# Kernel tuning notes

Measured on AMD Instinct MI355X. Metric: run time of the kernel, lower is better.

The kernel has to match this reference:

```python
import jax, jax.numpy as jnp
import numpy as np
from math import pi

RADIUS = 40.0  # radius_scale
B, N = 1, 512


def map_polar_sqr(x, y, eps=1e-9):
    r = jnp.sqrt(x * x + y * y + eps)
    cond1 = (x == 0.0) & (y == 0.0)
    cond2 = (jnp.abs(y) <= jnp.abs(x)) & (~cond1)
    sx = jnp.where(x == 0.0, 1.0, x)  # safe denominators
    sy = jnp.where(y == 0.0, 1.0, y)
    c = 4.0 / pi
    x2 = jnp.sign(x) * r
    y2 = c * jnp.sign(x) * r * jnp.arctan(y / sx)
    x3 = c * jnp.sign(y) * r * jnp.arctan(x / sy)
    y3 = jnp.sign(y) * r
    x_out = jnp.where(cond1, 0.0, jnp.where(cond2, x2, x3))
    y_out = jnp.where(cond1, 0.0, jnp.where(cond2, y2, y3))
    return x_out, y_out


def axis_weights(g, size):
    # F.grid_sample bilinear, align_corners=False, padding_mode='zeros':
    # pixel coord = ((g+1)*size - 1)/2; linear weights on floor/floor+1,
    # out-of-range taps drop to zero automatically (idx only covers 0..size-1).
    c = ((g + 1.0) * size - 1.0) * 0.5
    i0 = jnp.floor(c)
    f = c - i0
    idx = jnp.arange(size, dtype=g.dtype)
    m0 = (idx == i0[..., None]).astype(g.dtype)
    m1 = (idx == i0[..., None] + 1.0).astype(g.dtype)
    return (1.0 - f)[..., None] * m0 + f[..., None] * m1  # [..., size]


def cts_conv(kernel, field, center, feat, mask, radius):
    # kernel: [o, i, kD, kH, kW]; field/center: [b, n/m, 3]; feat: [b, n, i]; mask: [b, n, 1]
    rel = (field[:, None] - center[:, :, None]) / radius            # [b,m,n,3]
    r2 = jnp.sum(rel * rel, -1)                                     # [b,m,n]
    att = jax.nn.relu((1.0 - r2) ** 3)[..., None] * mask[:, None]   # [b,m,n,1]
    xs, ys = map_polar_sqr(rel[..., 0], rel[..., 1])
    zs = rel[..., 2]
    kD, kH, kW = kernel.shape[2:]
    # grid_sample coord order: grid x -> W (last dim), y -> H, z -> D (first spatial dim)
    wz = axis_weights(zs, kD)
    wy = axis_weights(ys, kH)
    wx = axis_weights(xs, kW)
    w = jnp.einsum('bmnz,bmny,bmnx->bmnzyx', wz, wy, wx)
    w = w.reshape(*w.shape[:3], -1)                                 # [b,m,n,g=kD*kH*kW]
    fa = feat[:, None] * att                                        # [b,m,n,i]
    # exact trilinear interp + neighbor contraction without the [b,m,n,o,i] tensor:
    t = jnp.einsum('bmng,bmni->bmgi', w, fa)                        # [b,m,g,i]
    K = kernel.reshape(kernel.shape[0], kernel.shape[1], -1)        # [o,i,g]
    return jnp.einsum('bmgi,oig->bmo', t, K)


def setup_inputs() -> dict:
    key = jax.random.key(0)
    ks = jax.random.split(key, 24)

    def kern(k, o, i):
        return (jax.random.uniform(k, (o, i, 4, 4, 4), dtype=jnp.float32) - 0.5) / float(np.sqrt(i))

    def lin(kw, kb, o, i):
        return (jax.random.normal(kw, (o, i), dtype=jnp.float32) * 0.05,
                jax.random.normal(kb, (o,), dtype=jnp.float32) * 0.05)

    p = jax.random.normal(ks[0], (B, N, 3), dtype=jnp.float32) * 20.0
    v = jax.random.normal(ks[1], (B, N, 3), dtype=jnp.float32)
    other_feats = jax.random.normal(ks[2], (B, N, 62), dtype=jnp.float32)
    fluid_mask = jnp.ones((B, N, 1), dtype=jnp.float32)

    k_fluid = kern(ks[3], 32, 66)
    Wf, bf = lin(ks[4], ks[5], 32, 66)
    k1 = kern(ks[6], 64, 64); W1, b1 = lin(ks[7], ks[8], 64, 64)
    k2 = kern(ks[9], 64, 64); W2, b2 = lin(ks[10], ks[11], 64, 64)
    k3 = kern(ks[12], 64, 64); W3, b3 = lin(ks[13], ks[14], 64, 64)
    k4 = kern(ks[15], 6, 64); W4, b4 = lin(ks[16], ks[17], 6, 64)
    return dict(p=p, v=v, other_feats=other_feats, fluid_mask=fluid_mask,
                k_fluid=k_fluid, Wf=Wf, bf=bf,
                k1=k1, W1=W1, b1=b1, k2=k2, W2=W2, b2=b2,
                k3=k3, W3=W3, b3=b3, k4=k4, W4=W4, b4=b4)


def reference(p, v, other_feats, fluid_mask, k_fluid, Wf, bf,
              k1, W1, b1, k2, W2, b2, k3, W3, b3, k4, W4, b4):
    feats0 = jnp.concatenate([jnp.ones_like(p[..., :1]), v, other_feats], -1)  # [b,n,66]
    oc = cts_conv(k_fluid, p, p, feats0, fluid_mask, RADIUS)
    od = feats0 @ Wf.T + bf
    output = jnp.concatenate([oc, od], -1)  # [b,n,64]
    for k, W, bb in ((k1, W1, b1), (k2, W2, b2), (k3, W3, b3), (k4, W4, b4)):
        h = jax.nn.relu(output)
        oc = cts_conv(k, p, p, h, fluid_mask, RADIUS)
        od = h @ W.T + bb
        if od.shape[-1] == output.shape[-1]:
            output = oc + od + output
        else:
            output = oc + od
    return output  # [b,n,6]
```

## Files before the change

kernel.cpp:

```cpp
#include <hip/hip_runtime.h>

typedef _Float16 f16;
typedef _Float16 f16x8 __attribute__((ext_vector_type(8)));
typedef float f32x4 __attribute__((ext_vector_type(4)));
typedef int iv2 __attribute__((ext_vector_type(2)));

#define INV_R (1.0f / 40.0f)
#define NBLK 512

#define F_BAR 0u
#define F_B0  2304u
#define F_K   2560u
#define F_HT  2286080u
#define F_T0  2695680u
#define F_T1  7119360u
#define F_T2  11379200u
#define F_T3  15639040u
#define F_T4  19898880u
#define F_OG  24158720u
#define NEED_FULL 24289792u

#define C_B0  2304u
#define C_K   2560u
#define C_HTA 2286080u
#define C_HTB 2368000u
#define C_TA  2449920u
#define C_TB  6873600u
#define C_OG  11133440u

#define K1_OFF 552960u
#define K2_OFF 1085440u
#define K3_OFF 1617920u
#define K4_OFF 2150400u

#define PREP_TOTAL 1231936

__device__ __forceinline__ void st_sys_u16(void* p, unsigned v) {
  asm volatile("global_store_short %0, %1, off sc0 sc1" :: "v"(p), "v"(v) : "memory");
}
__device__ __forceinline__ void st_sys_f32(float* p, float v) {
  asm volatile("global_store_dword %0, %1, off sc0 sc1" :: "v"(p), "v"(v) : "memory");
}
__device__ __forceinline__ void st_sys_b64(void* p, iv2 v) {
  asm volatile("global_store_dwordx2 %0, %1, off sc0 sc1" :: "v"(p), "v"(v) : "memory");
}
__device__ __forceinline__ unsigned f16bits(float x) {
  union { f16 h; unsigned short s; } cv; cv.h = (f16)x; return (unsigned)cv.s;
}

__device__ __forceinline__ unsigned bar_ld(unsigned* p) {
  return __hip_atomic_load(p, __ATOMIC_RELAXED, __HIP_MEMORY_SCOPE_AGENT);
}
__device__ void gridbar(unsigned* bar, int phase) {
  asm volatile("s_waitcnt vmcnt(0)" ::: "memory");
  __syncthreads();
  if (threadIdx.x == 0) {
    int bid = blockIdx.x;
    int xcd = bid & 7;
    unsigned* xcnt = bar + xcd * 32 + phase;
    unsigned* xrel = bar + 256 + xcd * 32 + phase;
    unsigned* gcnt = bar + 512 + phase;
    unsigned* grel = bar + 544 + phase;
    __hip_atomic_fetch_add(xcnt, 1u, __ATOMIC_RELAXED, __HIP_MEMORY_SCOPE_AGENT);
    if (bid < 8) {
      while (bar_ld(xcnt) < (NBLK / 8)) __builtin_amdgcn_s_sleep(2);
      __hip_atomic_fetch_add(gcnt, 1u, __ATOMIC_RELAXED, __HIP_MEMORY_SCOPE_AGENT);
      if (bid == 0) {
        while (bar_ld(gcnt) < 8u) __builtin_amdgcn_s_sleep(2);
        __hip_atomic_store(grel, 1u, __ATOMIC_RELAXED, __HIP_MEMORY_SCOPE_AGENT);
      } else {
        while (bar_ld(grel) == 0u) __builtin_amdgcn_s_sleep(4);
      }
      __hip_atomic_store(xrel, 1u, __ATOMIC_RELAXED, __HIP_MEMORY_SCOPE_AGENT);
    } else {
      while (bar_ld(xrel) == 0u) __builtin_amdgcn_s_sleep(64);
    }
    asm volatile("" ::: "memory");
  }
  __syncthreads();
}

__device__ __forceinline__ float feats0_val(int ch, int n, const float* v, const float* other) {
  if (ch == 0) return 1.0f;
  if (ch < 4) return v[n * 3 + (ch - 1)];
  return other[n * 62 + (ch - 4)];
}
__device__ __forceinline__ float atan_poly(float t) {
  float t2 = t * t;
  float p = -0.0117212f;
  p = p * t2 + 0.05265332f;
  p = p * t2 - 0.11643287f;
  p = p * t2 + 0.19354346f;
  p = p * t2 - 0.33262347f;
  p = p * t2 + 0.99997726f;
  return t * p;
}
__device__ __forceinline__ void axis_w(float g, int& i0c, int& i1c, float& w0, float& w1) {
  float c = 2.0f * g + 1.5f;
  float fl = floorf(c);
  float f = c - fl;
  int i0 = (int)fl;
  w0 = (i0 >= 0 && i0 <= 3) ? (1.0f - f) : 0.0f;
  w1 = (i0 >= -1 && i0 <= 2) ? f : 0.0f;
  i0c = min(max(i0, 0), 3);
  i1c = min(max(i0 + 1, 0), 3);
}

__device__ void prep_body(const float* __restrict__ v, const float* __restrict__ other,
                          const float* __restrict__ kf, const float* __restrict__ Wf,
                          const float* __restrict__ bf,
                          const float* __restrict__ k1, const float* __restrict__ W1,
                          const float* __restrict__ k2, const float* __restrict__ W2,
                          const float* __restrict__ k3, const float* __restrict__ W3,
                          const float* __restrict__ k4, const float* __restrict__ W4,
                          f16* __restrict__ K0, float* __restrict__ B0,
                          f16* __restrict__ hT0, f16* __restrict__ t0) {
  for (int idx = blockIdx.x * 256 + threadIdx.x; idx < PREP_TOTAL; idx += NBLK * 256) {
    int e = idx;
    if (e < 40960) {
      int i = e >> 9, n = e & 511;
      float val = (i < 66) ? feats0_val(i, n, v, other) : 0.0f;
      st_sys_u16(hT0 + e, f16bits(val));
      continue;
    }
    e -= 40960;
    if (e < 49152) {
      int m = e / 96, j = e % 96;
      float val = (j < 66) ? feats0_val(j, m, v, other) : 0.0f;
      st_sys_u16(t0 + (size_t)m * 4320 + 4224 + j, f16bits(val));
      continue;
    }
    e -= 49152;
    if (e < 276480) {
      int o = e / 4320, k = e % 4320;
      float val = 0.0f;
      if (o < 32) { if (k < 4224) val = kf[o * 4224 + k]; }
      else if (k >= 4224 && k < 4290) val = Wf[(o - 32) * 66 + (k - 4224)];
      st_sys_u16(K0 + e, f16bits(val));
      continue;
    }
    e -= 276480;
    if (e < 798720) {
      int which = e / 266240, ee = e % 266240;
      const float* kk = which == 0 ? k1 : (which == 1 ? k2 : k3);
      const float* WW = which == 0 ? W1 : (which == 1 ? W2 : W3);
      int o = ee / 4160, k = ee % 4160;
      float val = (k < 4096) ? kk[o * 4096 + k] : WW[o * 64 + (k - 4096)];
      st_sys_u16(K0 + (K1_OFF / 2) + (size_t)which * 266240 + ee, f16bits(val));
      continue;
    }
    e -= 798720;
    if (e < 66560) {
      int o = e / 4160, k = e % 4160;
      float val = 0.0f;
      if (o < 6) val = (k < 4096) ? k4[o * 4096 + k] : W4[o * 64 + (k - 4096)];
      st_sys_u16(K0 + (K4_OFF / 2) + e, f16bits(val));
      continue;
    }
    e -= 66560;
    if (e < 64) st_sys_f32(&B0[e], (e < 32) ? 0.0f : bf[e - 32]);
  }
}

template<int CI, int ITILES, int KDIM>
__device__ void stage1_body(const float* __restrict__ p, const float* __restrict__ mask,
                            const f16* __restrict__ hT_in, f16* __restrict__ tout,
                            f16* __restrict__ Wl) {
  const int tid = threadIdx.x;
  const int m = blockIdx.x;
  const int wave = tid >> 6, lane = tid & 63;
  const int row = lane & 15, kgrp = lane >> 4;
  const int grow = wave * 16 + row;

  const float pmx = p[m * 3 + 0], pmy = p[m * 3 + 1], pmz = p[m * 3 + 2];
  f32x4 acc[ITILES];
  #pragma unroll
  for (int it = 0; it < ITILES; ++it) acc[it] = f32x4{0.f, 0.f, 0.f, 0.f};

  #pragma unroll
  for (int half = 0; half < 2; ++half) {
    __syncthreads();
    int4* w4 = (int4*)Wl;
    int4 z4 = make_int4(0, 0, 0, 0);
    #pragma unroll
    for (int i = 0; i < 8; ++i) w4[tid + i * 256] = z4;
    __syncthreads();
    {
      const int n = half * 256 + tid;
      float x = (p[n * 3 + 0] - pmx) * INV_R;
      float y = (p[n * 3 + 1] - pmy) * INV_R;
      float z = (p[n * 3 + 2] - pmz) * INV_R;
      float r2 = x * x + y * y + z * z;
      float q = 1.0f - r2;
      float att = (q > 0.0f) ? q * q * q * mask[n] : 0.0f;
      bool c1 = (x == 0.0f) && (y == 0.0f);
      bool c2 = (fabsf(y) <= fabsf(x)) && !c1;
      float r = sqrtf(x * x + y * y + 1e-9f);
      float num = c2 ? y : x;
      float den = c2 ? x : y;
      float a = atan_poly(num / den);
      float s2 = copysignf(r, x), s3 = copysignf(r, y);
      const float C4PI = 1.2732395447351628f;
      float xs = c1 ? 0.0f : (c2 ? s2 : C4PI * s3 * a);
      float ys = c1 ? 0.0f : (c2 ? C4PI * s2 * a : s3);
      float zs = z;
      int iz0, iz1, iy0, iy1, ix0, ix1;
      float wz0, wz1, wy0, wy1, wx0, wx1;
      axis_w(zs, iz0, iz1, wz0, wz1);
      axis_w(ys, iy0, iy1, wy0, wy1);
      axis_w(xs, ix0, ix1, wx0, wx1);
      wz0 *= att; wz1 *= att;
      int gz[2] = {iz0 * 16, iz1 * 16};
      int gy[2] = {iy0 * 4, iy1 * 4};
      int gx[2] = {ix0, ix1};
      float wzv[2] = {wz0, wz1}, wyv[2] = {wy0, wy1}, wxv[2] = {wx0, wx1};
      #pragma unroll
      for (int za = 0; za < 2; ++za)
        #pragma unroll
        for (int ya = 0; ya < 2; ++ya)
          #pragma unroll
          for (int xa = 0; xa < 2; ++xa) {
            float w = wzv[za] * wyv[ya] * wxv[xa];
            if (w != 0.0f) {
              int g = gz[za] + gy[ya] + gx[xa];
              Wl[g * 256 + (tid ^ ((g & 7) << 3))] = (f16)w;
            }
          }
    }
    __syncthreads();
    #pragma unroll
    for (int k0 = 0; k0 < 8; ++k0) {
      const int n0l = k0 * 32 + kgrp * 8;
      f16x8 afrag = *(f16x8*)&Wl[grow * 256 + (n0l ^ ((grow & 7) << 3))];
      f16x8 bfr[ITILES];
      #pragma unroll
      for (int it = 0; it < ITILES; ++it)
        bfr[it] = *(const f16x8*)&hT_in[(it * 16 + row) * 512 + half * 256 + n0l];
      #pragma unroll
      for (int it = 0; it < ITILES; ++it)
        acc[it] = __builtin_amdgcn_mfma_f32_16x16x32_f16(afrag, bfr[it], acc[it], 0, 0, 0);
    }
  }
  const int g4 = wave * 16 + kgrp * 4;
  #pragma unroll
  for (int it = 0; it < ITILES; ++it) {
    const int icol = it * 16 + row;
    if (icol < CI) {
      union { f16 h[4]; iv2 i; } cv;
      #pragma unroll
      for (int r = 0; r < 4; ++r) cv.h[r] = (f16)acc[it][r];
      st_sys_b64(&tout[(size_t)m * KDIM + icol * 64 + g4], cv.i);
    }
  }
}

template<int KDIM, bool RES, bool FINAL>
__device__ void stage2_body(const f16* __restrict__ t, const f16* __restrict__ Kf,
                            const float* __restrict__ bias, float* __restrict__ outG,
                            f16* __restrict__ hT_out, f16* __restrict__ tnext,
                            float* __restrict__ dout, float* __restrict__ red) {
  int b = blockIdx.x;
  if (b >= 128) return;
  int mtile = b >> 2, otile = b & 3;
  constexpr int KSTEPS = KDIM / 32;
  int tid = threadIdx.x;
  int kpart = tid >> 6, lane = tid & 63;
  int row = lane & 15, kgrp = lane >> 4;
  int mrow = mtile * 16 + row;
  int ocol = otile * 16 + row;
  f32x4 acc = {0.f, 0.f, 0.f, 0.f};
  for (int ks = kpart; ks < KSTEPS; ks += 4) {
    int k0 = ks * 32 + kgrp * 8;
    f16x8 afrag = *(const f16x8*)&t[(size_t)mrow * KDIM + k0];
    f16x8 bfrag = *(const f16x8*)&Kf[(size_t)ocol * KDIM + k0];
    acc = __builtin_amdgcn_mfma_f32_16x16x32_f16(afrag, bfrag, acc, 0, 0, 0);
  }
  if (kpart > 0) {
    #pragma unroll
    for (int r = 0; r < 4; ++r)
      red[(kpart - 1) * 256 + (kgrp * 4 + r) * 16 + row] = acc[r];
  }
  __syncthreads();
  if (kpart == 0) {
    #pragma unroll
    for (int kw = 0; kw < 3; ++kw)
      #pragma unroll
      for (int r = 0; r < 4; ++r)
        acc[r] += red[kw * 256 + (kgrp * 4 + r) * 16 + row];
    #pragma unroll
    for (int r = 0; r < 4; ++r) {
      int mm = mtile * 16 + kgrp * 4 + r;
      int oo = otile * 16 + row;
      if (FINAL) {
        if (oo < 6) dout[mm * 6 + oo] = acc[r] + bias[oo];
      } else {
        float val = acc[r] + bias[oo];
        if (RES) val += outG[mm * 64 + oo];
        outG[mm * 64 + oo] = val;
        float h = fmaxf(val, 0.0f);
        unsigned hb = f16bits(h);
        st_sys_u16(&hT_out[oo * 512 + mm], hb);
        st_sys_u16(&tnext[(size_t)mm * 4160 + 4096 + oo], hb);
      }
    }
  }
}

__global__ __launch_bounds__(256, 2) void mega_kernel(
    const float* p, const float* v, const float* other, const float* mask,
    const float* kf, const float* Wf, const float* bf,
    const float* k1, const float* W1, const float* b1,
    const float* k2, const float* W2, const float* b2,
    const float* k3, const float* W3, const float* b3,
    const float* k4, const float* W4, const float* b4,
    float* dout, char* ws) {
  __shared__ int4 blob[2048];
  f16* Wl = (f16*)blob;
  float* red = (float*)blob;
  unsigned* bar = (unsigned*)(ws + F_BAR);

  f16* K0  = (f16*)(ws + F_K);
  float* B0 = (float*)(ws + F_B0);
  f16* hT0 = (f16*)(ws + F_HT);
  f16* hT1 = hT0 + 40960;
  f16* hT2 = hT0 + 81920;
  f16* hT3 = hT0 + 122880;
  f16* hT4 = hT0 + 163840;
  f16* t0 = (f16*)(ws + F_T0);
  f16* t1 = (f16*)(ws + F_T1);
  f16* t2 = (f16*)(ws + F_T2);
  f16* t3 = (f16*)(ws + F_T3);
  f16* t4 = (f16*)(ws + F_T4);
  float* outG = (float*)(ws + F_OG);

  prep_body(v, other, kf, Wf, bf, k1, W1, k2, W2, k3, W3, k4, W4, K0, B0, hT0, t0);
  gridbar(bar, 0);
  stage1_body<66, 5, 4320>(p, mask, hT0, t0, Wl);
  gridbar(bar, 1);
  stage2_body<4320, false, false>(t0, K0, B0, outG, hT1, t1, nullptr, red);
  gridbar(bar, 2);
  stage1_body<64, 4, 4160>(p, mask, hT1, t1, Wl);
  gridbar(bar, 3);
  stage2_body<4160, true, false>(t1, K0 + K1_OFF / 2, b1, outG, hT2, t2, nullptr, red);
  gridbar(bar, 4);
  stage1_body<64, 4, 4160>(p, mask, hT2, t2, Wl);
  gridbar(bar, 5);
  stage2_body<4160, true, false>(t2, K0 + K2_OFF / 2, b2, outG, hT3, t3, nullptr, red);
  gridbar(bar, 6);
  stage1_body<64, 4, 4160>(p, mask, hT3, t3, Wl);
  gridbar(bar, 7);
  stage2_body<4160, true, false>(t3, K0 + K3_OFF / 2, b3, outG, hT4, t4, nullptr, red);
  gridbar(bar, 8);
  stage1_body<64, 4, 4160>(p, mask, hT4, t4, Wl);
  gridbar(bar, 9);
  stage2_body<4160, false, true>(t4, K0 + K4_OFF / 2, b4, outG, nullptr, nullptr, dout, red);
}

__global__ __launch_bounds__(256) void prep_g(
    const float* v, const float* other, const float* kf, const float* Wf, const float* bf,
    const float* k1, const float* W1, const float* k2, const float* W2,
    const float* k3, const float* W3, const float* k4, const float* W4,
    f16* K0, float* B0, f16* hT0, f16* t0) {
  prep_body(v, other, kf, Wf, bf, k1, W1, k2, W2, k3, W3, k4, W4, K0, B0, hT0, t0);
}
template<int CI, int ITILES, int KDIM>
__global__ __launch_bounds__(256) void stage1_g(const float* p, const float* mask,
                                                const f16* hT_in, f16* tout) {
  __shared__ int4 blob[2048];
  stage1_body<CI, ITILES, KDIM>(p, mask, hT_in, tout, (f16*)blob);
}
template<int KDIM, bool RES, bool FINAL>
__global__ __launch_bounds__(256) void stage2_g(const f16* t, const f16* Kf,
                                                const float* bias, float* outG,
                                                f16* hT_out, f16* tnext, float* dout) {
  __shared__ float red[3 * 256];
  stage2_body<KDIM, RES, FINAL>(t, Kf, bias, outG, hT_out, tnext, dout, red);
}

extern "C" void kernel_launch(void* const* d_in, const int* in_sizes, int n_in,
                              void* d_out, int out_size, void* d_ws, size_t ws_size,
                              hipStream_t stream) {
  const float* p     = (const float*)d_in[0];
  const float* v     = (const float*)d_in[1];
  const float* other = (const float*)d_in[2];
  const float* mask  = (const float*)d_in[3];
  const float* kf    = (const float*)d_in[4];
  const float* Wf    = (const float*)d_in[5];
  const float* bf    = (const float*)d_in[6];
  const float* k1    = (const float*)d_in[7];
  const float* W1    = (const float*)d_in[8];
  const float* b1    = (const float*)d_in[9];
  const float* k2    = (const float*)d_in[10];
  const float* W2    = (const float*)d_in[11];
  const float* b2    = (const float*)d_in[12];
  const float* k3    = (const float*)d_in[13];
  const float* W3    = (const float*)d_in[14];
  const float* b3    = (const float*)d_in[15];
  const float* k4    = (const float*)d_in[16];
  const float* W4    = (const float*)d_in[17];
  const float* b4    = (const float*)d_in[18];
  float* dout = (float*)d_out;
  char* ws = (char*)d_ws;
  (void)in_sizes; (void)n_in; (void)out_size;

  int maxb = 0;
  hipError_t e1 = hipOccupancyMaxActiveBlocksPerMultiprocessor(
      &maxb, (const void*)mega_kernel, 256, 0);
  if (e1 == hipSuccess && maxb >= 2 && ws_size >= NEED_FULL) {
    hipMemsetAsync(ws + F_BAR, 0, 2304, stream);
    void* args[] = {
      (void*)&p, (void*)&v, (void*)&other, (void*)&mask,
      (void*)&kf, (void*)&Wf, (void*)&bf,
      (void*)&k1, (void*)&W1, (void*)&b1,
      (void*)&k2, (void*)&W2, (void*)&b2,
      (void*)&k3, (void*)&W3, (void*)&b3,
      (void*)&k4, (void*)&W4, (void*)&b4,
      (void*)&dout, (void*)&ws
    };
    hipError_t e2 = hipLaunchCooperativeKernel((const void*)mega_kernel, dim3(NBLK),
                                               dim3(256), args, 0, stream);
    if (e2 == hipSuccess) return;
  }

  f16* K0  = (f16*)(ws + C_K);
  float* B0 = (float*)(ws + C_B0);
  f16* hTA = (f16*)(ws + C_HTA);
  f16* hTB = (f16*)(ws + C_HTB);
  f16* tA  = (f16*)(ws + C_TA);
  f16* tB  = (f16*)(ws + C_TB);
  float* outG = (float*)(ws + C_OG);

  prep_g<<<NBLK, 256, 0, stream>>>(v, other, kf, Wf, bf, k1, W1, k2, W2, k3, W3, k4, W4,
                                   K0, B0, hTA, tA);
  stage1_g<66, 5, 4320><<<NBLK, 256, 0, stream>>>(p, mask, hTA, tA);
  stage2_g<4320, false, false><<<128, 256, 0, stream>>>(tA, K0, B0, outG, hTB, tB, nullptr);
  stage1_g<64, 4, 4160><<<NBLK, 256, 0, stream>>>(p, mask, hTB, tB);
  stage2_g<4160, true, false><<<128, 256, 0, stream>>>(tB, K0 + K1_OFF / 2, b1, outG, hTA, tA, nullptr);
  stage1_g<64, 4, 4160><<<NBLK, 256, 0, stream>>>(p, mask, hTA, tA);
  stage2_g<4160, true, false><<<128, 256, 0, stream>>>(tA, K0 + K2_OFF / 2, b2, outG, hTB, tB, nullptr);
  stage1_g<64, 4, 4160><<<NBLK, 256, 0, stream>>>(p, mask, hTB, tB);
  stage2_g<4160, true, false><<<128, 256, 0, stream>>>(tB, K0 + K3_OFF / 2, b3, outG, hTA, tA, nullptr);
  stage1_g<64, 4, 4160><<<NBLK, 256, 0, stream>>>(p, mask, hTA, tA);
  stage2_g<4160, false, true><<<128, 256, 0, stream>>>(tA, K0 + K4_OFF / 2, b4, outG, nullptr, nullptr, dout);
}
```

Baseline: 190.2 us.

## Remap stage work by hardware XCC id so intermediates stay in local L2

Each block reads its XCC id from a hardware register and takes a per-XCC rank through an atomic counter. Stage1 rows and stage2 tiles are then assigned so that a stage2 block consumes only t rows produced on the same XCC. When that mapping holds, t writes use plain cached stores instead of system-coherent sc0 sc1 stores, which should cut L2 writeback traffic. If any XCC gets more than 64 blocks, every block falls back to the old blockIdx mapping; the shared memory blob is also doubled, which may affect occupancy.

Result: no change. 190.5 us (+0.2%).

```diff
diff --git a/kernel.cpp b/kernel.cpp
--- a/kernel.cpp
+++ b/kernel.cpp
@@ -8,17 +8,18 @@
 #define INV_R (1.0f / 40.0f)
 #define NBLK 512
 
-#define F_BAR 0u
-#define F_B0  2304u
-#define F_K   2560u
-#define F_HT  2286080u
-#define F_T0  2695680u
-#define F_T1  7119360u
-#define F_T2  11379200u
-#define F_T3  15639040u
-#define F_T4  19898880u
-#define F_OG  24158720u
-#define NEED_FULL 24289792u
+#define F_BAR  0u
+#define F_SELF 2304u
+#define F_B0   2368u
+#define F_K    2624u
+#define F_HT   2286144u
+#define F_T0   2695744u
+#define F_T1   7119424u
+#define F_T2   11379264u
+#define F_T3   15639104u
+#define F_T4   19898944u
+#define F_OG   24158784u
+#define NEED_FULL 24289856u
 
 #define C_B0  2304u
 #define C_K   2560u
@@ -56,9 +57,9 @@
   __syncthreads();
   if (threadIdx.x == 0) {
     int bid = blockIdx.x;
-    int xcd = bid & 7;
-    unsigned* xcnt = bar + xcd * 32 + phase;
-    unsigned* xrel = bar + 256 + xcd * 32 + phase;
+    int cls = bid & 7;
+    unsigned* xcnt = bar + cls * 32 + phase;
+    unsigned* xrel = bar + 256 + cls * 32 + phase;
     unsigned* gcnt = bar + 512 + phase;
     unsigned* grel = bar + 544 + phase;
     __hip_atomic_fetch_add(xcnt, 1u, __ATOMIC_RELAXED, __HIP_MEMORY_SCOPE_AGENT);
@@ -165,9 +166,8 @@
 template<int CI, int ITILES, int KDIM>
 __device__ void stage1_body(const float* __restrict__ p, const float* __restrict__ mask,
                             const f16* __restrict__ hT_in, f16* __restrict__ tout,
-                            f16* __restrict__ Wl) {
+                            f16* __restrict__ Wl, int m, bool local) {
   const int tid = threadIdx.x;
-  const int m = blockIdx.x;
   const int wave = tid >> 6, lane = tid & 63;
   const int row = lane & 15, kgrp = lane >> 4;
   const int grow = wave * 16 + row;
@@ -246,10 +246,12 @@
   for (int it = 0; it < ITILES; ++it) {
     const int icol = it * 16 + row;
     if (icol < CI) {
-      union { f16 h[4]; iv2 i; } cv;
+      union { f16 h[4]; iv2 i; short4 s; } cv;
       #pragma unroll
       for (int r = 0; r < 4; ++r) cv.h[r] = (f16)acc[it][r];
-      st_sys_b64(&tout[(size_t)m * KDIM + icol * 64 + g4], cv.i);
+      f16* dst = &tout[(size_t)m * KDIM + icol * 64 + g4];
+      if (local) *(short4*)dst = cv.s;
+      else st_sys_b64(dst, cv.i);
     }
   }
 }
@@ -258,15 +260,14 @@
 __device__ void stage2_body(const f16* __restrict__ t, const f16* __restrict__ Kf,
                             const float* __restrict__ bias, float* __restrict__ outG,
                             f16* __restrict__ hT_out, f16* __restrict__ tnext,
-                            float* __restrict__ dout, float* __restrict__ red) {
-  int b = blockIdx.x;
-  if (b >= 128) return;
-  int mtile = b >> 2, otile = b & 3;
+                            float* __restrict__ dout, float* __restrict__ red,
+                            bool active, int mbase, int otile, bool local) {
+  if (!active) return;
   constexpr int KSTEPS = KDIM / 32;
   int tid = threadIdx.x;
   int kpart = tid >> 6, lane = tid & 63;
   int row = lane & 15, kgrp = lane >> 4;
-  int mrow = mtile * 16 + row;
+  int mrow = mbase + row;
   int ocol = otile * 16 + row;
   f32x4 acc = {0.f, 0.f, 0.f, 0.f};
   for (int ks = kpart; ks < KSTEPS; ks += 4) {
@@ -289,8 +290,8 @@
         acc[r] += red[kw * 256 + (kgrp * 4 + r) * 16 + row];
     #pragma unroll
     for (int r = 0; r < 4; ++r) {
-      int mm = mtile * 16 + kgrp * 4 + r;
-      int oo = otile * 16 + row;
+      int mm = mbase + kgrp * 4 + r;
+      int oo = ocol;
       if (FINAL) {
         if (oo < 6) dout[mm * 6 + oo] = acc[r] + bias[oo];
       } else {
@@ -300,7 +301,9 @@
         float h = fmaxf(val, 0.0f);
         unsigned hb = f16bits(h);
         st_sys_u16(&hT_out[oo * 512 + mm], hb);
-        st_sys_u16(&tnext[(size_t)mm * 4160 + 4096 + oo], hb);
+        f16* tp = &tnext[(size_t)mm * 4160 + 4096 + oo];
+        if (local) { union { unsigned short u; f16 f; } c; c.u = (unsigned short)hb; *tp = c.f; }
+        else st_sys_u16(tp, hb);
       }
     }
   }
@@ -314,10 +317,24 @@
     const float* k3, const float* W3, const float* b3,
     const float* k4, const float* W4, const float* b4,
     float* dout, char* ws) {
-  __shared__ int4 blob[2048];
+  __shared__ int4 blob[4096];
+  __shared__ unsigned s_rank;
   f16* Wl = (f16*)blob;
   float* red = (float*)blob;
   unsigned* bar = (unsigned*)(ws + F_BAR);
+  unsigned* selfcnt = (unsigned*)(ws + F_SELF);
+  unsigned* ovp = selfcnt + 8;
+
+  unsigned xcc;
+  asm volatile("s_getreg_b32 %0, hwreg(20, 0, 32)" : "=s"(xcc));
+  xcc &= 7u;
+  if (threadIdx.x == 0) {
+    unsigned r = atomicAdd(&selfcnt[xcc], 1u);
+    if (r >= 64u) __hip_atomic_store(ovp, 1u, __ATOMIC_RELAXED, __HIP_MEMORY_SCOPE_AGENT);
+    s_rank = r;
+  }
+  __syncthreads();
+  unsigned rank = s_rank;
 
   f16* K0  = (f16*)(ws + F_K);
   float* B0 = (float*)(ws + F_B0);
@@ -335,25 +352,33 @@
 
   prep_body(v, other, kf, Wf, bf, k1, W1, k2, W2, k3, W3, k4, W4, K0, B0, hT0, t0);
   gridbar(bar, 0);
-  stage1_body<66, 5, 4320>(p, mask, hT0, t0, Wl);
+
+  bool local = (__hip_atomic_load(ovp, __ATOMIC_RELAXED, __HIP_MEMORY_SCOPE_AGENT) == 0u);
+  int m1    = local ? (int)(xcc * 64u + rank) : (int)blockIdx.x;
+  bool s2a  = local ? (rank < 16u) : (blockIdx.x < 128);
+  int tix   = local ? (int)rank : (int)blockIdx.x;
+  int ot    = tix & 3;
+  int mbase = local ? (int)(xcc * 64u + (rank >> 2) * 16u) : ((int)(blockIdx.x >> 2) * 16);
+
+  stage1_body<66, 5, 4320>(p, mask, hT0, t0, Wl, m1, local);
   gridbar(bar, 1);
-  stage2_body<4320, false, false>(t0, K0, B0, outG, hT1, t1, nullptr, red);
+  stage2_body<4320, false, false>(t0, K0, B0, outG, hT1, t1, nullptr, red, s2a, mbase, ot, local);
   gridbar(bar, 2);
-  stage1_body<64, 4, 4160>(p, mask, hT1, t1, Wl);
+  stage1_body<64, 4, 4160>(p, mask, hT1, t1, Wl, m1, local);
   gridbar(bar, 3);
-  stage2_body<4160, true, false>(t1, K0 + K1_OFF / 2, b1, outG, hT2, t2, nullptr, red);
+  stage2_body<4160, true, false>(t1, K0 + K1_OFF / 2, b1, outG, hT2, t2, nullptr, red, s2a, mbase, ot, local);
   gridbar(bar, 4);
-  stage1_body<64, 4, 4160>(p, mask, hT2, t2, Wl);
+  stage1_body<64, 4, 4160>(p, mask, hT2, t2, Wl, m1, local);
   gridbar(bar, 5);
-  stage2_body<4160, true, false>(t2, K0 + K2_OFF / 2, b2, outG, hT3, t3, nullptr, red);
+  stage2_body<4160, true, false>(t2, K0 + K2_OFF / 2, b2, outG, hT3, t3, nullptr, red, s2a, mbase, ot, local);
   gridbar(bar, 6);
-  stage1_body<64, 4, 4160>(p, mask, hT3, t3, Wl);
+  stage1_body<64, 4, 4160>(p, mask, hT3, t3, Wl, m1, local);
   gridbar(bar, 7);
-  stage2_body<4160, true, false>(t3, K0 + K3_OFF / 2, b3, outG, hT4, t4, nullptr, red);
+  stage2_body<4160, true, false>(t3, K0 + K3_OFF / 2, b3, outG, hT4, t4, nullptr, red, s2a, mbase, ot, local);
   gridbar(bar, 8);
-  stage1_body<64, 4, 4160>(p, mask, hT4, t4, Wl);
+  stage1_body<64, 4, 4160>(p, mask, hT4, t4, Wl, m1, local);
   gridbar(bar, 9);
-  stage2_body<4160, false, true>(t4, K0 + K4_OFF / 2, b4, outG, nullptr, nullptr, dout, red);
+  stage2_body<4160, false, true>(t4, K0 + K4_OFF / 2, b4, outG, nullptr, nullptr, dout, red, s2a, mbase, ot, local);
 }
 
 __global__ __launch_bounds__(256) void prep_g(
@@ -367,14 +392,16 @@
 __global__ __launch_bounds__(256) void stage1_g(const float* p, const float* mask,
                                                 const f16* hT_in, f16* tout) {
   __shared__ int4 blob[2048];
-  stage1_body<CI, ITILES, KDIM>(p, mask, hT_in, tout, (f16*)blob);
+  stage1_body<CI, ITILES, KDIM>(p, mask, hT_in, tout, (f16*)blob, blockIdx.x, false);
 }
 template<int KDIM, bool RES, bool FINAL>
 __global__ __launch_bounds__(256) void stage2_g(const f16* t, const f16* Kf,
                                                 const float* bias, float* outG,
                                                 f16* hT_out, f16* tnext, float* dout) {
   __shared__ float red[3 * 256];
-  stage2_body<KDIM, RES, FINAL>(t, Kf, bias, outG, hT_out, tnext, dout, red);
+  stage2_body<KDIM, RES, FINAL>(t, Kf, bias, outG, hT_out, tnext, dout, red,
+                                blockIdx.x < 128, ((int)blockIdx.x >> 2) * 16,
+                                (int)blockIdx.x & 3, false);
 }
 
 extern "C" void kernel_launch(void* const* d_in, const int* in_sizes, int n_in,
@@ -407,7 +434,7 @@
   hipError_t e1 = hipOccupancyMaxActiveBlocksPerMultiprocessor(
       &maxb, (const void*)mega_kernel, 256, 0);
   if (e1 == hipSuccess && maxb >= 2 && ws_size >= NEED_FULL) {
-    hipMemsetAsync(ws + F_BAR, 0, 2304, stream);
+    hipMemsetAsync(ws, 0, 2368, stream);
     void* args[] = {
       (void*)&p, (void*)&v, (void*)&other, (void*)&mask,
       (void*)&kf, (void*)&Wf, (void*)&bf,
```
